# Kernel optimization log

Hardware: AMD Instinct MI355X
Metric: run time of the kernel (lower is better)

The kernel has to match this reference:

```python
import jax, jax.numpy as jnp
import numpy as np

B, C, E = 4, 2048, 1024
H, D = 16, 64  # num_heads, head_size

def setup_inputs() -> dict:
    key = jax.random.key(0)
    kx, kk, kq, kv, ko = jax.random.split(key, 5)
    s = 1.0 / np.sqrt(E)
    so = 1.0 / np.sqrt(H * D)
    return {
        "x": jax.random.normal(kx, (B, C, E), dtype=jnp.float32),
        "Wk": jax.random.uniform(kk, (H * D, E), jnp.float32, -s, s),
        "Wq": jax.random.uniform(kq, (H * D, E), jnp.float32, -s, s),
        "Wv": jax.random.uniform(kv, (H * D, E), jnp.float32, -s, s),
        "Wo": jax.random.uniform(ko, (E, H * D), jnp.float32, -so, so),
    }

def reference(x, Wk, Wq, Wv, Wo):
    b, c, e = x.shape
    # projections -> [B, H, C, D]
    def proj(W):
        return (x @ W.T).reshape(b, c, H, D).transpose(0, 2, 1, 3)
    k = proj(Wk)
    q = proj(Wq)
    v = proj(Wv)
    # scores [B, H, C, C]; mask applied before scaling (as in source; -inf*scale = -inf)
    sa = jnp.einsum("bhqd,bhkd->bhqk", q, k)
    mask = ~jnp.tril(jnp.ones((c, c), dtype=bool))  # True above diagonal
    masked = jnp.where(mask, -jnp.inf, sa)
    scale = 1.0 / np.sqrt(D)
    attn = jax.nn.softmax(masked * scale, axis=-1)
    out = jnp.einsum("bhqk,bhkd->bhqd", attn, v)  # [B, H, C, D]
    flat = out.transpose(0, 2, 1, 3).reshape(b, c, H * D)
    return flat @ Wo.T
```

## Files before the change

### kernel.cpp

```cpp
#include <hip/hip_runtime.h>
#include <hip/hip_bf16.h>

typedef __bf16 bf16x8 __attribute__((ext_vector_type(8)));
typedef __bf16 bf16x4 __attribute__((ext_vector_type(4)));
typedef float f32x4 __attribute__((ext_vector_type(4)));

#define NEG_INF (-__builtin_inff())

__global__ void cvt_f32_bf16(const float* __restrict__ src, __bf16* __restrict__ dst, int n) {
    int idx = blockIdx.x * blockDim.x + threadIdx.x;
    int stride = gridDim.x * blockDim.x;
    for (int i = idx * 4; i < n; i += stride * 4) {
        float4 v = *(const float4*)(src + i);
        bf16x4 o;
        o[0] = (__bf16)v.x; o[1] = (__bf16)v.y; o[2] = (__bf16)v.z; o[3] = (__bf16)v.w;
        *(bf16x4*)(dst + i) = o;
    }
}

template <int MODE>
__launch_bounds__(256, 3)
__global__ void gemm_bt(const __bf16* __restrict__ A, const __bf16* __restrict__ Bm,
                        void* __restrict__ Out, int M, int N, int K) {
    __shared__ __align__(1024) char smem[32768];
    const int tid = threadIdx.x;
    const int w = tid >> 6, lane = tid & 63;
    const int lr = lane & 15, lg = lane >> 4;
    const int wm0 = (w >> 1) * 64, wn0 = (w & 1) * 64;

    const int nbx = gridDim.x;
    int id = blockIdx.y * nbx + blockIdx.x;
    int q8 = (nbx * gridDim.y) >> 3;
    int vid = (id & 7) * q8 + (id >> 3);
    const int m0 = (vid / nbx) * 128, n0 = (vid % nbx) * 128;

    const char* Ab = (const char*)A;
    const char* Bb = (const char*)Bm;

    f32x4 acc[4][4] = {};

    const int s_row_in_chunk = lane >> 3;
    const int s_col16 = lane & 7;

    const int nt = K >> 6;
    for (int t = 0; t < nt; ++t) {
#pragma unroll
        for (int r = 0; r < 4; ++r) {
            int c = w * 4 + r;
            int row = c * 8 + s_row_in_chunk;
            const char* srcA = Ab + ((size_t)(m0 + row) * K + t * 64) * 2 + s_col16 * 16;
            const char* srcB = Bb + ((size_t)(n0 + row) * K + t * 64) * 2 + s_col16 * 16;
            __builtin_amdgcn_global_load_lds(
                (const __attribute__((address_space(1))) void*)srcA,
                (__attribute__((address_space(3))) void*)(smem + c * 1024), 16, 0, 0);
            __builtin_amdgcn_global_load_lds(
                (const __attribute__((address_space(1))) void*)srcB,
                (__attribute__((address_space(3))) void*)(smem + 16384 + c * 1024), 16, 0, 0);
        }
        __syncthreads();

#pragma unroll
        for (int kk = 0; kk < 2; ++kk) {
            bf16x8 af[4], bf[4];
#pragma unroll
            for (int mi = 0; mi < 4; ++mi)
                af[mi] = *(const bf16x8*)(smem + (wm0 + mi * 16 + lr) * 128 + kk * 64 + lg * 16);
#pragma unroll
            for (int ni = 0; ni < 4; ++ni)
                bf[ni] = *(const bf16x8*)(smem + 16384 + (wn0 + ni * 16 + lr) * 128 + kk * 64 + lg * 16);
            __builtin_amdgcn_s_setprio(1);
#pragma unroll
            for (int mi = 0; mi < 4; ++mi)
#pragma unroll
                for (int ni = 0; ni < 4; ++ni)
                    acc[mi][ni] = __builtin_amdgcn_mfma_f32_16x16x32_bf16(
                        af[mi], bf[ni], acc[mi][ni], 0, 0, 0);
            __builtin_amdgcn_s_setprio(0);
        }
        __syncthreads();
    }

#pragma unroll
    for (int mi = 0; mi < 4; ++mi)
#pragma unroll
        for (int ni = 0; ni < 4; ++ni)
#pragma unroll
            for (int r = 0; r < 4; ++r) {
                int m = m0 + wm0 + mi * 16 + lg * 4 + r;
                int n = n0 + wn0 + ni * 16 + lr;
                float v = acc[mi][ni][r];
                if (MODE == 0) {
                    int proj = n >> 10, nn = n & 1023;
                    int h = nn >> 6, d = nn & 63;
                    int bb = m >> 11, c = m & 2047;
                    if (proj == 2) {
                        ((__bf16*)Out)[(size_t)2 * 8388608 +
                                       ((size_t)((bb * 16 + h) * 64 + d)) * 2048 + c] = (__bf16)v;
                    } else {
                        float scale = (proj == 0) ? 0.125f : 1.0f;
                        ((__bf16*)Out)[(size_t)proj * 8388608 +
                                       ((size_t)(bb * 16 + h) * 2048 + c) * 64 + d] =
                            (__bf16)(v * scale);
                    }
                } else {
                    ((float*)Out)[(size_t)m * N + n] = v;
                }
            }
}

__device__ __forceinline__ unsigned swz(unsigned d) {
    return d ^ (((d >> 7) & 7) << 4);
}

__launch_bounds__(256, 4)
__global__ void attn_fwd(const __bf16* __restrict__ Q, const __bf16* __restrict__ K,
                         const __bf16* __restrict__ Vt, __bf16* __restrict__ Aout) {
    __shared__ char smem[40960];
    const int id = blockIdx.x;
    const int vid = (id & 7) * 128 + (id >> 3);
    const int bh = vid >> 4, pr = vid & 15;
    const int w = threadIdx.x >> 6, lane = threadIdx.x & 63;
    const int lr = lane & 15, lg = lane >> 4;
    const char* Kb  = (const char*)(K  + (size_t)bh * 2048 * 64);
    const char* Vtb = (const char*)(Vt + (size_t)bh * 64 * 2048);
    const __bf16* Qb = Q + (size_t)bh * 2048 * 64;
    const int b = bh >> 4, h = bh & 15;
    char* Pb = smem + 32768 + w * 2048;

    for (int pass = 0; pass < 2; ++pass) {
        const int qt = pass ? pr : 31 - pr;
        const int q0 = qt * 64 + w * 16;
        const int nt = qt + 1;

        bf16x8 qf[2];
#pragma unroll
        for (int kk = 0; kk < 2; ++kk)
            qf[kk] = *(const bf16x8*)&Qb[(size_t)(q0 + lr) * 64 + kk * 32 + lg * 8];

        f32x4 o[4] = {};
        float m = NEG_INF, l = 0.f;

        __syncthreads();
        {
            char* kd = smem;
            char* vd = smem + 16384;
#pragma unroll
            for (int i = 0; i < 2; ++i) {
                unsigned c = (unsigned)(w * 2 + i);
                unsigned d = c * 1024 + (unsigned)lane * 16;
                unsigned bs = swz(d);
                __builtin_amdgcn_global_load_lds(
                    (const __attribute__((address_space(1))) void*)(Kb + bs),
                    (__attribute__((address_space(3))) void*)(kd + c * 1024), 16, 0, 0);
                unsigned row = bs >> 7, colb = bs & 127;
                __builtin_amdgcn_global_load_lds(
                    (const __attribute__((address_space(1))) void*)(Vtb + (size_t)row * 4096 + colb),
                    (__attribute__((address_space(3))) void*)(vd + c * 1024), 16, 0, 0);
            }
        }

        for (int t = 0; t < nt; ++t) {
            __syncthreads();
            if (t + 1 < nt) {
                char* kd = smem + ((t + 1) & 1) * 8192;
                char* vd = smem + 16384 + ((t + 1) & 1) * 8192;
#pragma unroll
                for (int i = 0; i < 2; ++i) {
                    unsigned c = (unsigned)(w * 2 + i);
                    unsigned d = c * 1024 + (unsigned)lane * 16;
                    unsigned bs = swz(d);
                    __builtin_amdgcn_global_load_lds(
                        (const __attribute__((address_space(1))) void*)(Kb + (size_t)(t + 1) * 8192 + bs),
                        (__attribute__((address_space(3))) void*)(kd + c * 1024), 16, 0, 0);
                    unsigned row = bs >> 7, colb = bs & 127;
                    __builtin_amdgcn_global_load_lds(
                        (const __attribute__((address_space(1))) void*)(Vtb + (size_t)row * 4096 +
                                                                       (size_t)(t + 1) * 128 + colb),
                        (__attribute__((address_space(3))) void*)(vd + c * 1024), 16, 0, 0);
                }
            }
            const char* Ks = smem + (t & 1) * 8192;
            const char* Vs = smem + 16384 + (t & 1) * 8192;
            const int k0 = t * 64;

            f32x4 s[4] = {};
#pragma unroll
            for (int kk = 0; kk < 2; ++kk)
#pragma unroll
                for (int sub = 0; sub < 4; ++sub) {
                    bf16x8 kf = *(const bf16x8*)(Ks + swz((unsigned)((sub * 16 + lr) * 128 + kk * 64 + lg * 16)));
                    s[sub] = __builtin_amdgcn_mfma_f32_16x16x32_bf16(kf, qf[kk], s[sub], 0, 0, 0);
                }
            if (t == qt) {
#pragma unroll
                for (int sub = 0; sub < 4; ++sub)
#pragma unroll
                    for (int r = 0; r < 4; ++r)
                        if (k0 + sub * 16 + lg * 4 + r > q0 + lr) s[sub][r] = NEG_INF;
            }
            float mloc = NEG_INF;
#pragma unroll
            for (int sub = 0; sub < 4; ++sub)
#pragma unroll
                for (int r = 0; r < 4; ++r) mloc = fmaxf(mloc, s[sub][r]);
            mloc = fmaxf(mloc, __shfl_xor(mloc, 16));
            mloc = fmaxf(mloc, __shfl_xor(mloc, 32));
            float mnew = fmaxf(m, mloc);
            float alpha = __expf(m - mnew);
            float rs = 0.f;
#pragma unroll
            for (int sub = 0; sub < 4; ++sub)
#pragma unroll
                for (int r = 0; r < 4; ++r) {
                    float p = __expf(s[sub][r] - mnew);
                    s[sub][r] = p;
                    rs += p;
                }
            rs += __shfl_xor(rs, 16);
            rs += __shfl_xor(rs, 32);
            l = l * alpha + rs;
            m = mnew;
#pragma unroll
            for (int ni = 0; ni < 4; ++ni) o[ni] *= alpha;

#pragma unroll
            for (int sub = 0; sub < 4; ++sub) {
                bf16x4 pk;
#pragma unroll
                for (int r = 0; r < 4; ++r) pk[r] = (__bf16)s[sub][r];
                *(bf16x4*)(Pb + swz((unsigned)(lr * 128 + sub * 32 + lg * 8))) = pk;
            }
            bf16x8 pfr[2];
#pragma unroll
            for (int kk = 0; kk < 2; ++kk)
                pfr[kk] = *(const bf16x8*)(Pb + swz((unsigned)(lr * 128 + kk * 64 + lg * 16)));

#pragma unroll
            for (int kk = 0; kk < 2; ++kk)
#pragma unroll
                for (int ni = 0; ni < 4; ++ni) {
                    bf16x8 vf = *(const bf16x8*)(Vs + swz((unsigned)((ni * 16 + lr) * 128 + kk * 64 + lg * 16)));
                    o[ni] = __builtin_amdgcn_mfma_f32_16x16x32_bf16(vf, pfr[kk], o[ni], 0, 0, 0);
                }
        }

        float rinv = 1.0f / l;
#pragma unroll
        for (int ni = 0; ni < 4; ++ni) {
            bf16x4 ov;
#pragma unroll
            for (int r = 0; r < 4; ++r) ov[r] = (__bf16)(o[ni][r] * rinv);
            *(bf16x4*)&Aout[((size_t)b * 2048 + q0 + lr) * 1024 + h * 64 + ni * 16 + lg * 4] = ov;
        }
    }
}

extern "C" void kernel_launch(void* const* d_in, const int* in_sizes, int n_in,
                              void* d_out, int out_size, void* d_ws, size_t ws_size,
                              hipStream_t stream) {
    const float* x  = (const float*)d_in[0];
    const float* Wk = (const float*)d_in[1];
    const float* Wq = (const float*)d_in[2];
    const float* Wv = (const float*)d_in[3];
    const float* Wo = (const float*)d_in[4];

    char* ws = (char*)d_ws;
    __bf16* xb   = (__bf16*)(ws);
    __bf16* wqkv = (__bf16*)(ws + 16777216);
    __bf16* wo_b = (__bf16*)(ws + 23068672);
    __bf16* qkv  = (__bf16*)(ws + 25165824);
    __bf16* aout = (__bf16*)(ws + 75497472);
    float* out = (float*)d_out;

    cvt_f32_bf16<<<2048, 256, 0, stream>>>(x, xb, 8388608);
    cvt_f32_bf16<<<1024, 256, 0, stream>>>(Wq, wqkv, 1048576);
    cvt_f32_bf16<<<1024, 256, 0, stream>>>(Wk, wqkv + 1048576, 1048576);
    cvt_f32_bf16<<<1024, 256, 0, stream>>>(Wv, wqkv + 2097152, 1048576);
    cvt_f32_bf16<<<1024, 256, 0, stream>>>(Wo, wo_b, 1048576);

    gemm_bt<0><<<dim3(24, 64), 256, 0, stream>>>(xb, wqkv, qkv, 8192, 3072, 1024);
    attn_fwd<<<dim3(1024), 256, 0, stream>>>(qkv, qkv + 8388608, qkv + 16777216, aout);
    gemm_bt<1><<<dim3(8, 64), 256, 0, stream>>>(aout, wo_b, out, 8192, 1024, 1024);
}
```

Before: 192.0 us.

## Use a dedicated 256x128-tile QKV GEMM with 512-thread blocks

Replaces the templated QKV projection GEMM with a dedicated kernel. It uses 256x128 output tiles and 8 waves per block, so each loaded weight tile serves twice as many rows of x, and it cuts the grid to 768 blocks. The output projection GEMM becomes a plain fp32-store kernel, and its occupancy hint rises from 3 to 4 blocks. The larger LDS footprint (48KB) and the aggressive launch-bounds hint of 6 blocks of 512 threads may constrain registers or occupancy.

```diff
diff --git a/kernel.cpp b/kernel.cpp
--- a/kernel.cpp
+++ b/kernel.cpp
@@ -18,10 +18,95 @@
     }
 }
 
-template <int MODE>
-__launch_bounds__(256, 3)
+__launch_bounds__(512, 6)
+__global__ void gemm_qkv(const __bf16* __restrict__ A, const __bf16* __restrict__ Bm,
+                         __bf16* __restrict__ Out, int M, int N, int K) {
+    __shared__ __align__(1024) char smem[49152];
+    const int tid = threadIdx.x;
+    const int w = tid >> 6, lane = tid & 63;
+    const int lr = lane & 15, lg = lane >> 4;
+    const int wm0 = (w >> 1) * 64, wn0 = (w & 1) * 64;
+
+    const int nbx = 24;
+    int id = blockIdx.x;
+    int q8 = (int)(gridDim.x) >> 3;
+    int vid = (id & 7) * q8 + (id >> 3);
+    const int m0 = (vid / nbx) * 256, n0 = (vid % nbx) * 128;
+
+    const char* Ab = (const char*)A;
+    const char* Bb = (const char*)Bm;
+
+    f32x4 acc[4][4] = {};
+
+    const int s_row8 = lane >> 3;
+    const int s_col16 = lane & 7;
+
+    const int nt = K >> 6;
+    for (int t = 0; t < nt; ++t) {
+#pragma unroll
+        for (int i = 0; i < 6; ++i) {
+            int c = w * 6 + i;
+            const char* src;
+            if (c < 32) {
+                int row = c * 8 + s_row8;
+                src = Ab + ((size_t)(m0 + row) * K + t * 64) * 2 + s_col16 * 16;
+            } else {
+                int row = (c - 32) * 8 + s_row8;
+                src = Bb + ((size_t)(n0 + row) * K + t * 64) * 2 + s_col16 * 16;
+            }
+            __builtin_amdgcn_global_load_lds(
+                (const __attribute__((address_space(1))) void*)src,
+                (__attribute__((address_space(3))) void*)(smem + c * 1024), 16, 0, 0);
+        }
+        __syncthreads();
+
+#pragma unroll
+        for (int kk = 0; kk < 2; ++kk) {
+            bf16x8 af[4], bf[4];
+#pragma unroll
+            for (int mi = 0; mi < 4; ++mi)
+                af[mi] = *(const bf16x8*)(smem + (wm0 + mi * 16 + lr) * 128 + kk * 64 + lg * 16);
+#pragma unroll
+            for (int ni = 0; ni < 4; ++ni)
+                bf[ni] = *(const bf16x8*)(smem + 32768 + (wn0 + ni * 16 + lr) * 128 + kk * 64 + lg * 16);
+            __builtin_amdgcn_s_setprio(1);
+#pragma unroll
+            for (int mi = 0; mi < 4; ++mi)
+#pragma unroll
+                for (int ni = 0; ni < 4; ++ni)
+                    acc[mi][ni] = __builtin_amdgcn_mfma_f32_16x16x32_bf16(
+                        af[mi], bf[ni], acc[mi][ni], 0, 0, 0);
+            __builtin_amdgcn_s_setprio(0);
+        }
+        __syncthreads();
+    }
+
+#pragma unroll
+    for (int mi = 0; mi < 4; ++mi)
+#pragma unroll
+        for (int ni = 0; ni < 4; ++ni)
+#pragma unroll
+            for (int r = 0; r < 4; ++r) {
+                int m = m0 + wm0 + mi * 16 + lg * 4 + r;
+                int n = n0 + wn0 + ni * 16 + lr;
+                float v = acc[mi][ni][r];
+                int proj = n >> 10, nn = n & 1023;
+                int h = nn >> 6, d = nn & 63;
+                int bb = m >> 11, c = m & 2047;
+                if (proj == 2) {
+                    Out[(size_t)2 * 8388608 +
+                        ((size_t)((bb * 16 + h) * 64 + d)) * 2048 + c] = (__bf16)v;
+                } else {
+                    float scale = (proj == 0) ? 0.125f : 1.0f;
+                    Out[(size_t)proj * 8388608 +
+                        ((size_t)(bb * 16 + h) * 2048 + c) * 64 + d] = (__bf16)(v * scale);
+                }
+            }
+}
+
+__launch_bounds__(256, 4)
 __global__ void gemm_bt(const __bf16* __restrict__ A, const __bf16* __restrict__ Bm,
-                        void* __restrict__ Out, int M, int N, int K) {
+                        float* __restrict__ Out, int M, int N, int K) {
     __shared__ __align__(1024) char smem[32768];
     const int tid = threadIdx.x;
     const int w = tid >> 6, lane = tid & 63;
@@ -39,7 +124,7 @@
 
     f32x4 acc[4][4] = {};
 
-    const int s_row_in_chunk = lane >> 3;
+    const int s_row8 = lane >> 3;
     const int s_col16 = lane & 7;
 
     const int nt = K >> 6;
@@ -47,7 +132,7 @@
 #pragma unroll
         for (int r = 0; r < 4; ++r) {
             int c = w * 4 + r;
-            int row = c * 8 + s_row_in_chunk;
+            int row = c * 8 + s_row8;
             const char* srcA = Ab + ((size_t)(m0 + row) * K + t * 64) * 2 + s_col16 * 16;
             const char* srcB = Bb + ((size_t)(n0 + row) * K + t * 64) * 2 + s_col16 * 16;
             __builtin_amdgcn_global_load_lds(
@@ -88,23 +173,7 @@
             for (int r = 0; r < 4; ++r) {
                 int m = m0 + wm0 + mi * 16 + lg * 4 + r;
                 int n = n0 + wn0 + ni * 16 + lr;
-                float v = acc[mi][ni][r];
-                if (MODE == 0) {
-                    int proj = n >> 10, nn = n & 1023;
-                    int h = nn >> 6, d = nn & 63;
-                    int bb = m >> 11, c = m & 2047;
-                    if (proj == 2) {
-                        ((__bf16*)Out)[(size_t)2 * 8388608 +
-                                       ((size_t)((bb * 16 + h) * 64 + d)) * 2048 + c] = (__bf16)v;
-                    } else {
-                        float scale = (proj == 0) ? 0.125f : 1.0f;
-                        ((__bf16*)Out)[(size_t)proj * 8388608 +
-                                       ((size_t)(bb * 16 + h) * 2048 + c) * 64 + d] =
-                            (__bf16)(v * scale);
-                    }
-                } else {
-                    ((float*)Out)[(size_t)m * N + n] = v;
-                }
+                Out[(size_t)m * N + n] = acc[mi][ni][r];
             }
 }
 
@@ -278,7 +347,7 @@
     cvt_f32_bf16<<<1024, 256, 0, stream>>>(Wv, wqkv + 2097152, 1048576);
     cvt_f32_bf16<<<1024, 256, 0, stream>>>(Wo, wo_b, 1048576);
 
-    gemm_bt<0><<<dim3(24, 64), 256, 0, stream>>>(xb, wqkv, qkv, 8192, 3072, 1024);
+    gemm_qkv<<<dim3(768), 512, 0, stream>>>(xb, wqkv, qkv, 8192, 3072, 1024);
     attn_fwd<<<dim3(1024), 256, 0, stream>>>(qkv, qkv + 8388608, qkv + 16777216, aout);
-    gemm_bt<1><<<dim3(8, 64), 256, 0, stream>>>(aout, wo_b, out, 8192, 1024, 1024);
-}
+    gemm_bt<<<dim3(8, 64), 256, 0, stream>>>(aout, wo_b, out, 8192, 1024, 1024);
+}
```

Result: slower. 626.2 us (+226.1%).

## Enlarge GEMM tiles to 256x128 with 512-thread blocks and fuse weight conversions

Applied to the files above, without the earlier changes.

The projection GEMMs now use 256x128 output tiles computed by 8 waves per block. A-tile rows are shared across more waves, which cuts B-operand reloads and gives more work per block. The four separate weight-conversion launches are merged into one kernel that picks its source by index. The trade-off is more LDS per block (48KB) and lower blocks-per-CU occupancy, plus a larger tail effect from fewer, bigger blocks.

```diff
diff --git a/kernel.cpp b/kernel.cpp
--- a/kernel.cpp
+++ b/kernel.cpp
@@ -18,44 +18,60 @@
     }
 }
 
+__global__ void cvt_weights(const float* __restrict__ Wq, const float* __restrict__ Wk,
+                            const float* __restrict__ Wv, const float* __restrict__ Wo,
+                            __bf16* __restrict__ wqkv, __bf16* __restrict__ wo_b) {
+    int i = (blockIdx.x * blockDim.x + threadIdx.x) * 4;
+    int sel = i >> 20;
+    int off = i & 1048575;
+    const float* src = (sel == 0) ? Wq : (sel == 1) ? Wk : (sel == 2) ? Wv : Wo;
+    __bf16* dst = (sel < 3) ? (wqkv + (size_t)sel * 1048576) : wo_b;
+    float4 v = *(const float4*)(src + off);
+    bf16x4 o;
+    o[0] = (__bf16)v.x; o[1] = (__bf16)v.y; o[2] = (__bf16)v.z; o[3] = (__bf16)v.w;
+    *(bf16x4*)(dst + off) = o;
+}
+
 template <int MODE>
-__launch_bounds__(256, 3)
-__global__ void gemm_bt(const __bf16* __restrict__ A, const __bf16* __restrict__ Bm,
+__launch_bounds__(512, 2)
+__global__ void gemm256(const __bf16* __restrict__ A, const __bf16* __restrict__ Bm,
                         void* __restrict__ Out, int M, int N, int K) {
-    __shared__ __align__(1024) char smem[32768];
+    __shared__ __align__(1024) char smem[49152];
     const int tid = threadIdx.x;
     const int w = tid >> 6, lane = tid & 63;
     const int lr = lane & 15, lg = lane >> 4;
     const int wm0 = (w >> 1) * 64, wn0 = (w & 1) * 64;
 
-    const int nbx = gridDim.x;
-    int id = blockIdx.y * nbx + blockIdx.x;
-    int q8 = (nbx * gridDim.y) >> 3;
+    const int nbx = N >> 7;
+    int id = blockIdx.x;
+    int q8 = (int)(gridDim.x) >> 3;
     int vid = (id & 7) * q8 + (id >> 3);
-    const int m0 = (vid / nbx) * 128, n0 = (vid % nbx) * 128;
+    const int m0 = (vid / nbx) * 256, n0 = (vid % nbx) * 128;
 
     const char* Ab = (const char*)A;
     const char* Bb = (const char*)Bm;
 
     f32x4 acc[4][4] = {};
 
-    const int s_row_in_chunk = lane >> 3;
+    const int s_row8 = lane >> 3;
     const int s_col16 = lane & 7;
 
     const int nt = K >> 6;
     for (int t = 0; t < nt; ++t) {
 #pragma unroll
-        for (int r = 0; r < 4; ++r) {
-            int c = w * 4 + r;
-            int row = c * 8 + s_row_in_chunk;
-            const char* srcA = Ab + ((size_t)(m0 + row) * K + t * 64) * 2 + s_col16 * 16;
-            const char* srcB = Bb + ((size_t)(n0 + row) * K + t * 64) * 2 + s_col16 * 16;
+        for (int i = 0; i < 6; ++i) {
+            int c = w * 6 + i;
+            const char* src;
+            if (c < 32) {
+                int row = c * 8 + s_row8;
+                src = Ab + ((size_t)(m0 + row) * K + t * 64) * 2 + s_col16 * 16;
+            } else {
+                int row = (c - 32) * 8 + s_row8;
+                src = Bb + ((size_t)(n0 + row) * K + t * 64) * 2 + s_col16 * 16;
+            }
             __builtin_amdgcn_global_load_lds(
-                (const __attribute__((address_space(1))) void*)srcA,
+                (const __attribute__((address_space(1))) void*)src,
                 (__attribute__((address_space(3))) void*)(smem + c * 1024), 16, 0, 0);
-            __builtin_amdgcn_global_load_lds(
-                (const __attribute__((address_space(1))) void*)srcB,
-                (__attribute__((address_space(3))) void*)(smem + 16384 + c * 1024), 16, 0, 0);
         }
         __syncthreads();
 
@@ -67,7 +83,7 @@
                 af[mi] = *(const bf16x8*)(smem + (wm0 + mi * 16 + lr) * 128 + kk * 64 + lg * 16);
 #pragma unroll
             for (int ni = 0; ni < 4; ++ni)
-                bf[ni] = *(const bf16x8*)(smem + 16384 + (wn0 + ni * 16 + lr) * 128 + kk * 64 + lg * 16);
+                bf[ni] = *(const bf16x8*)(smem + 32768 + (wn0 + ni * 16 + lr) * 128 + kk * 64 + lg * 16);
             __builtin_amdgcn_s_setprio(1);
 #pragma unroll
             for (int mi = 0; mi < 4; ++mi)
@@ -273,12 +289,9 @@
     float* out = (float*)d_out;
 
     cvt_f32_bf16<<<2048, 256, 0, stream>>>(x, xb, 8388608);
-    cvt_f32_bf16<<<1024, 256, 0, stream>>>(Wq, wqkv, 1048576);
-    cvt_f32_bf16<<<1024, 256, 0, stream>>>(Wk, wqkv + 1048576, 1048576);
-    cvt_f32_bf16<<<1024, 256, 0, stream>>>(Wv, wqkv + 2097152, 1048576);
-    cvt_f32_bf16<<<1024, 256, 0, stream>>>(Wo, wo_b, 1048576);
-
-    gemm_bt<0><<<dim3(24, 64), 256, 0, stream>>>(xb, wqkv, qkv, 8192, 3072, 1024);
+    cvt_weights<<<4096, 256, 0, stream>>>(Wq, Wk, Wv, Wo, wqkv, wo_b);
+
+    gemm256<0><<<dim3(768), 512, 0, stream>>>(xb, wqkv, qkv, 8192, 3072, 1024);
     attn_fwd<<<dim3(1024), 256, 0, stream>>>(qkv, qkv + 8388608, qkv + 16777216, aout);
-    gemm_bt<1><<<dim3(8, 64), 256, 0, stream>>>(aout, wo_b, out, 8192, 1024, 1024);
-}
+    gemm256<1><<<dim3(256), 512, 0, stream>>>(aout, wo_b, out, 8192, 1024, 1024);
+}
```

Result: slower. 218.3 us (+13.7%).

## Double-buffer LDS tiles in projection GEMMs and merge weight conversion launches

Applied to the files above, without the earlier changes.

The GEMM kernel now uses two 32KB LDS buffers. It issues the global-to-LDS loads for the next K tile before computing on the current one, and drops the trailing barrier so there is one sync per iteration. This is meant to overlap memory latency with MFMA work, at the cost of doubling LDS use and lowering the occupancy hint from 3 to 2 blocks per CU. The four separate weight fp32-to-bf16 conversion launches are also merged into one kernel that selects the source by index, to cut launch overhead.

```diff
diff --git a/kernel.cpp b/kernel.cpp
--- a/kernel.cpp
+++ b/kernel.cpp
@@ -18,11 +18,25 @@
     }
 }
 
+__global__ void cvt_weights(const float* __restrict__ Wq, const float* __restrict__ Wk,
+                            const float* __restrict__ Wv, const float* __restrict__ Wo,
+                            __bf16* __restrict__ wqkv, __bf16* __restrict__ wo_b) {
+    int i = (blockIdx.x * blockDim.x + threadIdx.x) * 4;
+    int sel = i >> 20;
+    int off = i & 1048575;
+    const float* src = (sel == 0) ? Wq : (sel == 1) ? Wk : (sel == 2) ? Wv : Wo;
+    __bf16* dst = (sel < 3) ? (wqkv + (size_t)sel * 1048576) : wo_b;
+    float4 v = *(const float4*)(src + off);
+    bf16x4 o;
+    o[0] = (__bf16)v.x; o[1] = (__bf16)v.y; o[2] = (__bf16)v.z; o[3] = (__bf16)v.w;
+    *(bf16x4*)(dst + off) = o;
+}
+
 template <int MODE>
-__launch_bounds__(256, 3)
-__global__ void gemm_bt(const __bf16* __restrict__ A, const __bf16* __restrict__ Bm,
+__launch_bounds__(256, 2)
+__global__ void gemm_db(const __bf16* __restrict__ A, const __bf16* __restrict__ Bm,
                         void* __restrict__ Out, int M, int N, int K) {
-    __shared__ __align__(1024) char smem[32768];
+    __shared__ __align__(1024) char smem[65536];
     const int tid = threadIdx.x;
     const int w = tid >> 6, lane = tid & 63;
     const int lr = lane & 15, lg = lane >> 4;
@@ -38,36 +52,41 @@
     const char* Bb = (const char*)Bm;
 
     f32x4 acc[4][4] = {};
-
-    const int s_row_in_chunk = lane >> 3;
+    const int s_row8 = lane >> 3;
     const int s_col16 = lane & 7;
 
-    const int nt = K >> 6;
-    for (int t = 0; t < nt; ++t) {
+    auto stage = [&](int t, int buf) {
+        char* base = smem + buf * 32768;
 #pragma unroll
         for (int r = 0; r < 4; ++r) {
             int c = w * 4 + r;
-            int row = c * 8 + s_row_in_chunk;
+            int row = c * 8 + s_row8;
             const char* srcA = Ab + ((size_t)(m0 + row) * K + t * 64) * 2 + s_col16 * 16;
             const char* srcB = Bb + ((size_t)(n0 + row) * K + t * 64) * 2 + s_col16 * 16;
             __builtin_amdgcn_global_load_lds(
                 (const __attribute__((address_space(1))) void*)srcA,
-                (__attribute__((address_space(3))) void*)(smem + c * 1024), 16, 0, 0);
+                (__attribute__((address_space(3))) void*)(base + c * 1024), 16, 0, 0);
             __builtin_amdgcn_global_load_lds(
                 (const __attribute__((address_space(1))) void*)srcB,
-                (__attribute__((address_space(3))) void*)(smem + 16384 + c * 1024), 16, 0, 0);
-        }
+                (__attribute__((address_space(3))) void*)(base + 16384 + c * 1024), 16, 0, 0);
+        }
+    };
+
+    const int nt = K >> 6;
+    stage(0, 0);
+    for (int t = 0; t < nt; ++t) {
         __syncthreads();
-
+        if (t + 1 < nt) stage(t + 1, (t + 1) & 1);
+        const char* base = smem + (t & 1) * 32768;
 #pragma unroll
         for (int kk = 0; kk < 2; ++kk) {
             bf16x8 af[4], bf[4];
 #pragma unroll
             for (int mi = 0; mi < 4; ++mi)
-                af[mi] = *(const bf16x8*)(smem + (wm0 + mi * 16 + lr) * 128 + kk * 64 + lg * 16);
+                af[mi] = *(const bf16x8*)(base + (wm0 + mi * 16 + lr) * 128 + kk * 64 + lg * 16);
 #pragma unroll
             for (int ni = 0; ni < 4; ++ni)
-                bf[ni] = *(const bf16x8*)(smem + 16384 + (wn0 + ni * 16 + lr) * 128 + kk * 64 + lg * 16);
+                bf[ni] = *(const bf16x8*)(base + 16384 + (wn0 + ni * 16 + lr) * 128 + kk * 64 + lg * 16);
             __builtin_amdgcn_s_setprio(1);
 #pragma unroll
             for (int mi = 0; mi < 4; ++mi)
@@ -77,7 +96,6 @@
                         af[mi], bf[ni], acc[mi][ni], 0, 0, 0);
             __builtin_amdgcn_s_setprio(0);
         }
-        __syncthreads();
     }
 
 #pragma unroll
@@ -273,12 +291,9 @@
     float* out = (float*)d_out;
 
     cvt_f32_bf16<<<2048, 256, 0, stream>>>(x, xb, 8388608);
-    cvt_f32_bf16<<<1024, 256, 0, stream>>>(Wq, wqkv, 1048576);
-    cvt_f32_bf16<<<1024, 256, 0, stream>>>(Wk, wqkv + 1048576, 1048576);
-    cvt_f32_bf16<<<1024, 256, 0, stream>>>(Wv, wqkv + 2097152, 1048576);
-    cvt_f32_bf16<<<1024, 256, 0, stream>>>(Wo, wo_b, 1048576);
-
-    gemm_bt<0><<<dim3(24, 64), 256, 0, stream>>>(xb, wqkv, qkv, 8192, 3072, 1024);
+    cvt_weights<<<4096, 256, 0, stream>>>(Wq, Wk, Wv, Wo, wqkv, wo_b);
+
+    gemm_db<0><<<dim3(24, 64), 256, 0, stream>>>(xb, wqkv, qkv, 8192, 3072, 1024);
     attn_fwd<<<dim3(1024), 256, 0, stream>>>(qkv, qkv + 8388608, qkv + 16777216, aout);
-    gemm_bt<1><<<dim3(8, 64), 256, 0, stream>>>(aout, wo_b, out, 8192, 1024, 1024);
-}
+    gemm_db<1><<<dim3(8, 64), 256, 0, stream>>>(aout, wo_b, out, 8192, 1024, 1024);
+}
```

New measurement: 193.2 us. Within noise of the previous version (+0.6%).
